# Kernel tuning notes

Hardware: AMD Instinct MI355X
Metric: run time of the kernel (lower is better)

Reference implementation:

```python
import jax, jax.numpy as jnp
import numpy as np

B, S, D, H, V, C = 4, 2048, 1024, 16, 32000, 10
FFN_DIM = 2 * D
HD = D // H
SCALE = float(np.sqrt(HD))


def _posenc(seq, d):
    pos = jnp.arange(seq, dtype=jnp.float32)[:, None]
    div = jnp.exp(jnp.arange(0, d, 2, dtype=jnp.float32) * (-np.log(10000.0) / d))
    pe = jnp.zeros((seq, d), dtype=jnp.float32)
    pe = pe.at[:, 0::2].set(jnp.sin(pos * div))
    pe = pe.at[:, 1::2].set(jnp.cos(pos * div))
    return pe


def _layernorm(x, g, b, eps=1e-5):
    mu = jnp.mean(x, axis=-1, keepdims=True)
    var = jnp.mean(jnp.square(x - mu), axis=-1, keepdims=True)
    return (x - mu) * jax.lax.rsqrt(var + eps) * g + b


def setup_inputs() -> dict:
    key = jax.random.key(0)
    ks = jax.random.split(key, 10)
    x_ids = jax.random.randint(ks[0], (B, S), 0, V, dtype=jnp.int64 if jax.config.jax_enable_x64 else jnp.int32)
    mask = jnp.ones((B, S), dtype=jnp.int32)
    emb = (jax.random.normal(ks[1], (V, D), jnp.float32) * 0.02).at[0].set(0.0)  # padding_idx=0
    qkv_w = jax.random.normal(ks[2], (3 * D, D), jnp.float32) * 0.02
    fc_w = jax.random.normal(ks[3], (D, D), jnp.float32) * 0.02
    fc_b = jnp.zeros((D,), jnp.float32)
    ln1_g = jnp.ones((D,), jnp.float32); ln1_b = jnp.zeros((D,), jnp.float32)
    ffn_w1 = jax.random.normal(ks[4], (FFN_DIM, D), jnp.float32) * 0.02
    ffn_b1 = jnp.zeros((FFN_DIM,), jnp.float32)
    ffn_w2 = jax.random.normal(ks[5], (D, FFN_DIM), jnp.float32) * 0.02
    ffn_b2 = jnp.zeros((D,), jnp.float32)
    ln2_g = jnp.ones((D,), jnp.float32); ln2_b = jnp.zeros((D,), jnp.float32)
    pr_w1 = jax.random.normal(ks[6], (D, D), jnp.float32) * 0.02
    pr_b1 = jnp.zeros((D,), jnp.float32)
    pr_w2 = jax.random.normal(ks[7], (C, D), jnp.float32) * 0.02
    pr_b2 = jnp.zeros((C,), jnp.float32)
    return dict(x_ids=x_ids, mask=mask, emb=emb, qkv_w=qkv_w, fc_w=fc_w, fc_b=fc_b,
                ln1_g=ln1_g, ln1_b=ln1_b, ffn_w1=ffn_w1, ffn_b1=ffn_b1,
                ffn_w2=ffn_w2, ffn_b2=ffn_b2, ln2_g=ln2_g, ln2_b=ln2_b,
                pr_w1=pr_w1, pr_b1=pr_b1, pr_w2=pr_w2, pr_b2=pr_b2)


def reference(x_ids, mask, emb, qkv_w, fc_w, fc_b, ln1_g, ln1_b,
              ffn_w1, ffn_b1, ffn_w2, ffn_b2, ln2_g, ln2_b,
              pr_w1, pr_b1, pr_w2, pr_b2):
    # embedding + absolute positional encoding
    x = emb[x_ids] + _posenc(S, D)  # [B,S,D]
    residual = x
    # multi-head attention (dropout is identity at eval)
    qkv = jnp.einsum('bsd,ed->bse', x, qkv_w)  # [B,S,3D]
    q, k, v = jnp.split(qkv, 3, axis=-1)
    q = q.reshape(B, S, H, HD)
    k = k.reshape(B, S, H, HD)
    v = v.reshape(B, S, H, HD)
    attn = jnp.einsum('bqhd,bkhd->bhqk', q, k) / SCALE  # [B,H,S,S]
    attn = jnp.where(mask[:, None, None, :] == 0, -jnp.inf, attn)
    attn = jax.nn.softmax(attn, axis=-1)
    o = jnp.einsum('bhqk,bkhd->bqhd', attn, v).reshape(B, S, D)
    o = jnp.einsum('bsd,ed->bse', o, fc_w) + fc_b
    x = _layernorm(o + residual, ln1_g, ln1_b)
    # FFN block (residual + LayerNorm inside)
    h = jax.nn.gelu(jnp.einsum('bsd,fd->bsf', x, ffn_w1) + ffn_b1, approximate=False)
    h = jnp.einsum('bsf,df->bsd', h, ffn_w2) + ffn_b2
    x = _layernorm(h + x, ln2_g, ln2_b)
    # masked max-pool over sequence
    x = jnp.where(mask[:, :, None] == 0, -jnp.inf, x).max(axis=1)  # [B,D]
    # prediction head
    h = jax.nn.gelu(x @ pr_w1.T + pr_b1, approximate=False)
    logits = h @ pr_w2.T + pr_b2  # [B,C]
    return logits
```

## Files before the change

### kernel.cpp

```cpp
#include <hip/hip_runtime.h>
#include <math.h>

#define B_   4
#define S_   2048
#define D_   1024
#define H_   16
#define HD_  64
#define C_   10
#define FFN_ 2048
#define M_   (B_ * S_)
#define D3_  (3 * D_)

typedef unsigned short u16;
typedef __bf16 bf16x8 __attribute__((ext_vector_type(8)));
typedef float  f32x4  __attribute__((ext_vector_type(4)));

__device__ __forceinline__ u16 f2bf(float f) {
  union { float f; unsigned u; } x; x.f = f;
  unsigned r = x.u + 0x7fffu + ((x.u >> 16) & 1u);
  return (u16)(r >> 16);
}
__device__ __forceinline__ unsigned pkbf(float a, float b) {
  union { float f; unsigned u; } x, y; x.f = a; y.f = b;
  return __builtin_amdgcn_perm(y.u + 0x8000u, x.u + 0x8000u, 0x07060302u);
}
__device__ __forceinline__ float gelu_f(float x) {
  return 0.5f * x * (1.f + erff(x * 0.70710678118654752440f));
}
__device__ __forceinline__ void gload_lds16(const void* g, void* l) {
  __builtin_amdgcn_global_load_lds(
      (const __attribute__((address_space(1))) unsigned int*)g,
      (__attribute__((address_space(3))) unsigned int*)l, 16, 0, 0);
}
__device__ __forceinline__ bf16x8 ldsfrag(const u16* buf, int rowbase, int fr, int kb) {
  return *(const bf16x8*)&buf[(rowbase + fr) * 64 + ((kb ^ (fr & 7)) << 3)];
}

__global__ __launch_bounds__(256) void cvt_kernel(const float* __restrict__ src,
                                                  u16* __restrict__ dst, int n) {
  const int i = (blockIdx.x * 256 + threadIdx.x) * 4;
  if (i >= n) return;
  f32x4 v = *(const f32x4*)&src[i];
  ushort4 o;
  o.x = f2bf(v[0]); o.y = f2bf(v[1]); o.z = f2bf(v[2]); o.w = f2bf(v[3]);
  *(ushort4*)&dst[i] = o;
}

__global__ __launch_bounds__(256) void embed_kernel(const int* __restrict__ ids,
                                                    const float* __restrict__ emb,
                                                    float* __restrict__ resid,
                                                    u16* __restrict__ xb) {
  const int m  = blockIdx.x;
  const int s  = m & (S_ - 1);
  const int id = ids[m];
  const int d0 = threadIdx.x * 4;
#pragma unroll
  for (int k = 0; k < 4; ++k) {
    const int d   = d0 + k;
    const float e = emb[(size_t)id * D_ + d];
    const float fr  = expf((float)(d & ~1) * (-9.210340371976184f / 1024.0f));
    const float ang = (float)s * fr;
    const float pe  = (d & 1) ? cosf(ang) : sinf(ang);
    const float v   = e + pe;
    resid[(size_t)m * D_ + d] = v;
    xb[(size_t)m * D_ + d]    = f2bf(v);
  }
}

template <int BIAS, int GELU, int OUTBF, int VSPLIT>
__global__ __launch_bounds__(256) void gemm_bt(const u16* __restrict__ A,
                                               const u16* __restrict__ W,
                                               const float* __restrict__ bias,
                                               float* __restrict__ outf,
                                               u16* __restrict__ outb,
                                               u16* __restrict__ vt,
                                               int M, int N, int K) {
  __shared__ u16 As[128 * 64];
  __shared__ u16 Bs[128 * 64];
  const int tid  = threadIdx.x;
  const int lane = tid & 63;
  const int w    = tid >> 6;
  const int bx   = blockIdx.x, by = blockIdx.y;
  const int l3   = lane >> 3;
  const int sb   = (lane & 7) ^ l3;
  const u16* Ag0 = A + (size_t)(by * 128 + w * 32 + l3) * K + sb * 8;
  const u16* Wg0 = W + (size_t)(bx * 128 + w * 32 + l3) * K + sb * 8;

  f32x4 acc[4][4] = {};
  const int wr  = (w & 1) * 64;
  const int wc  = (w >> 1) * 64;
  const int fr  = lane & 15;
  const int fq  = lane >> 4;

  for (int kt = 0; kt < K; kt += 64) {
#pragma unroll
    for (int c = 0; c < 4; ++c) {
      gload_lds16(Ag0 + (size_t)(c * 8) * K + kt, &As[(w * 32 + c * 8) * 64]);
      gload_lds16(Wg0 + (size_t)(c * 8) * K + kt, &Bs[(w * 32 + c * 8) * 64]);
    }
    __syncthreads();
#pragma unroll
    for (int ks = 0; ks < 2; ++ks) {
      const int kb = ks * 4 + fq;
      bf16x8 af[4], bfr[4];
#pragma unroll
      for (int i = 0; i < 4; ++i) af[i] = ldsfrag(As, wr + i * 16, fr, kb);
#pragma unroll
      for (int j = 0; j < 4; ++j) bfr[j] = ldsfrag(Bs, wc + j * 16, fr, kb);
#pragma unroll
      for (int i = 0; i < 4; ++i)
#pragma unroll
        for (int j = 0; j < 4; ++j)
          acc[i][j] = __builtin_amdgcn_mfma_f32_16x16x32_bf16(af[i], bfr[j], acc[i][j], 0, 0, 0);
    }
    __syncthreads();
  }

  const int er = fq * 4;
  const int ec = fr;
  if (VSPLIT && bx >= 16) {
#pragma unroll
    for (int i = 0; i < 4; ++i) {
      const int gm0 = by * 128 + wr + i * 16 + er;
      const int bb  = gm0 >> 11;
      const int s0  = gm0 & (S_ - 1);
#pragma unroll
      for (int j = 0; j < 4; ++j) {
        const int dcol = bx * 128 + wc + j * 16 + ec - 2 * D_;
        const int hh = dcol >> 6, dd = dcol & 63;
        ushort4 pk;
        pk.x = f2bf(acc[i][j][0]); pk.y = f2bf(acc[i][j][1]);
        pk.z = f2bf(acc[i][j][2]); pk.w = f2bf(acc[i][j][3]);
        *(ushort4*)&vt[((size_t)((bb * H_ + hh) * 64 + dd)) * S_ + s0] = pk;
      }
    }
    return;
  }
#pragma unroll
  for (int i = 0; i < 4; ++i) {
#pragma unroll
    for (int j = 0; j < 4; ++j) {
      const int gn = bx * 128 + wc + j * 16 + ec;
      const float bv = BIAS ? bias[gn] : 0.f;
#pragma unroll
      for (int r = 0; r < 4; ++r) {
        const int gm = by * 128 + wr + i * 16 + er + r;
        float v = acc[i][j][r] + bv;
        if (GELU) v = gelu_f(v);
        if (OUTBF) outb[(size_t)gm * N + gn] = f2bf(v);
        else       outf[(size_t)gm * N + gn] = v;
      }
    }
  }
}

#define EXPSCL 0.18033688011112042f

__global__ __launch_bounds__(256) void attn_mfma_kernel(const u16* __restrict__ qkv,
                                                        const u16* __restrict__ vt,
                                                        const int* __restrict__ mask,
                                                        u16* __restrict__ attno) {
  __shared__ u16 Qs[128 * 64];
  __shared__ u16 Ks[64 * 64];
  __shared__ u16 Vts[64 * 64];
  __shared__ u16 Ps[4][32 * 64];
  __shared__ float mb[64];
  const int tid = threadIdx.x, lane = tid & 63, w = tid >> 6;
  const int id = blockIdx.x;
  const int qt = (id >> 3) & 15;
  const int bh = (id & 7) * 8 + (id >> 7);
  const int b = bh >> 4, h = bh & 15;
  const int l3 = lane >> 3;
  const int sb = (lane & 7) ^ l3;
  const int fr = lane & 15, fq = lane >> 4;

  {
    const u16* qbase = qkv + (size_t)(b * S_ + qt * 128 + w * 32) * D3_ + h * 64 + sb * 8;
#pragma unroll
    for (int c = 0; c < 4; ++c)
      gload_lds16(qbase + (size_t)(c * 8 + l3) * D3_, &Qs[(w * 32 + c * 8) * 64]);
  }

  float m_st[2] = {-3e38f, -3e38f};
  float l_st[2] = {0.f, 0.f};
  f32x4 ot[4][2] = {};
  u16* PsW = Ps[w];

  for (int kt = 0; kt < S_ / 64; ++kt) {
    __syncthreads();
    {
      const u16* kbase = qkv + (size_t)(b * S_ + kt * 64 + w * 16) * D3_ + D_ + h * 64 + sb * 8;
      gload_lds16(kbase + (size_t)l3 * D3_, &Ks[(w * 16) * 64]);
      gload_lds16(kbase + (size_t)(8 + l3) * D3_, &Ks[(w * 16 + 8) * 64]);
      const u16* vbase = vt + ((size_t)((b * H_ + h) * 64 + w * 16)) * S_ + kt * 64 + sb * 8;
      gload_lds16(vbase + (size_t)l3 * S_, &Vts[(w * 16) * 64]);
      gload_lds16(vbase + (size_t)(8 + l3) * S_, &Vts[(w * 16 + 8) * 64]);
    }
    if (tid < 64) mb[tid] = (mask[b * S_ + kt * 64 + tid] != 0) ? 0.f : -1e30f;
    __syncthreads();

    f32x4 sf[4][2] = {};
#pragma unroll
    for (int ks = 0; ks < 2; ++ks) {
      const int kb = ks * 4 + fq;
      bf16x8 qf0 = ldsfrag(Qs, w * 32, fr, kb);
      bf16x8 qf1 = ldsfrag(Qs, w * 32 + 16, fr, kb);
#pragma unroll
      for (int r4 = 0; r4 < 4; ++r4) {
        bf16x8 kf = ldsfrag(Ks, r4 * 16, fr, kb);
        sf[r4][0] = __builtin_amdgcn_mfma_f32_16x16x32_bf16(kf, qf0, sf[r4][0], 0, 0, 0);
        sf[r4][1] = __builtin_amdgcn_mfma_f32_16x16x32_bf16(kf, qf1, sf[r4][1], 0, 0, 0);
      }
    }
#pragma unroll
    for (int r4 = 0; r4 < 4; ++r4) {
      const f32x4 vb = *(const f32x4*)&mb[r4 * 16 + fq * 4];
      sf[r4][0] += vb;
      sf[r4][1] += vb;
    }

#pragma unroll
    for (int i = 0; i < 2; ++i) {
      float mt = fmaxf(fmaxf(fmaxf(sf[0][i][0], sf[0][i][1]), fmaxf(sf[0][i][2], sf[0][i][3])),
                 fmaxf(fmaxf(fmaxf(sf[1][i][0], sf[1][i][1]), fmaxf(sf[1][i][2], sf[1][i][3])),
                 fmaxf(fmaxf(fmaxf(sf[2][i][0], sf[2][i][1]), fmaxf(sf[2][i][2], sf[2][i][3])),
                       fmaxf(fmaxf(sf[3][i][0], sf[3][i][1]), fmaxf(sf[3][i][2], sf[3][i][3])))));
      mt = fmaxf(mt, __shfl_xor(mt, 16));
      mt = fmaxf(mt, __shfl_xor(mt, 32));
      const float mo = m_st[i];
      const float mn = fmaxf(mo, mt);
      const float alpha = __builtin_exp2f((mo - mn) * EXPSCL);
      const int prow = i * 16 + fr;
      u16* pw = PsW + prow * 64;
      float sum = 0.f;
#pragma unroll
      for (int r4 = 0; r4 < 4; ++r4) {
        const float p0 = __builtin_exp2f((sf[r4][i][0] - mn) * EXPSCL);
        const float p1 = __builtin_exp2f((sf[r4][i][1] - mn) * EXPSCL);
        const float p2 = __builtin_exp2f((sf[r4][i][2] - mn) * EXPSCL);
        const float p3 = __builtin_exp2f((sf[r4][i][3] - mn) * EXPSCL);
        sum += (p0 + p1) + (p2 + p3);
        const int bk0 = 2 * r4 + (fq >> 1);
        const int off = ((bk0 ^ (prow & 7)) << 3) + ((fq & 1) << 2);
        uint2 pk; pk.x = pkbf(p0, p1); pk.y = pkbf(p2, p3);
        *(uint2*)&pw[off] = pk;
      }
      sum += __shfl_xor(sum, 16);
      sum += __shfl_xor(sum, 32);
      l_st[i] = l_st[i] * alpha + sum;
      m_st[i] = mn;
#pragma unroll
      for (int db = 0; db < 4; ++db) ot[db][i] *= alpha;
    }
    asm volatile("s_waitcnt lgkmcnt(0)" ::: "memory");

#pragma unroll
    for (int ks = 0; ks < 2; ++ks) {
      const int kb = ks * 4 + fq;
      bf16x8 pf0 = ldsfrag(PsW, 0, fr, kb);
      bf16x8 pf1 = ldsfrag(PsW, 16, fr, kb);
#pragma unroll
      for (int db = 0; db < 4; ++db) {
        bf16x8 vf = ldsfrag(Vts, db * 16, fr, kb);
        ot[db][0] = __builtin_amdgcn_mfma_f32_16x16x32_bf16(vf, pf0, ot[db][0], 0, 0, 0);
        ot[db][1] = __builtin_amdgcn_mfma_f32_16x16x32_bf16(vf, pf1, ot[db][1], 0, 0, 0);
      }
    }
  }

#pragma unroll
  for (int i = 0; i < 2; ++i) {
    const float l = l_st[i];
    const float inv = (l > 0.f) ? 1.f / l : 0.f;
    const int qrow = qt * 128 + w * 32 + i * 16 + fr;
    u16* dst = attno + (size_t)(b * S_ + qrow) * D_ + h * 64 + fq * 4;
#pragma unroll
    for (int db = 0; db < 4; ++db) {
      ushort4 pk;
      pk.x = f2bf(ot[db][i][0] * inv);
      pk.y = f2bf(ot[db][i][1] * inv);
      pk.z = f2bf(ot[db][i][2] * inv);
      pk.w = f2bf(ot[db][i][3] * inv);
      *(ushort4*)&dst[db * 16] = pk;
    }
  }
}

__global__ __launch_bounds__(256) void ln_kernel(const float* __restrict__ a,
                                                 const float* __restrict__ res,
                                                 const float* __restrict__ g,
                                                 const float* __restrict__ be,
                                                 float* __restrict__ outf,
                                                 u16* __restrict__ outb) {
  const int row = blockIdx.x, tid = threadIdx.x;
  const int lane = tid & 63, w = tid >> 6;
  const size_t base = (size_t)row * D_ + tid * 4;
  const f32x4 va = *(const f32x4*)(a + base);
  const f32x4 vr = *(const f32x4*)(res + base);
  const f32x4 v  = va + vr;
  float s = v[0] + v[1] + v[2] + v[3];
#pragma unroll
  for (int o = 32; o > 0; o >>= 1) s += __shfl_xor(s, o);
  __shared__ float red[8];
  if (lane == 0) red[w] = s;
  __syncthreads();
  const float mu = (red[0] + red[1] + red[2] + red[3]) * (1.f / D_);
  const f32x4 d = v - mu;
  float s2 = d[0] * d[0] + d[1] * d[1] + d[2] * d[2] + d[3] * d[3];
#pragma unroll
  for (int o = 32; o > 0; o >>= 1) s2 += __shfl_xor(s2, o);
  if (lane == 0) red[4 + w] = s2;
  __syncthreads();
  const float var = (red[4] + red[5] + red[6] + red[7]) * (1.f / D_);
  const float rs = rsqrtf(var + 1e-5f);
#pragma unroll
  for (int k = 0; k < 4; ++k) {
    const int ch = tid * 4 + k;
    const float y = d[k] * rs * g[ch] + be[ch];
    outf[base + k] = y;
    outb[base + k] = f2bf(y);
  }
}

__global__ __launch_bounds__(256) void pool_part_kernel(const float* __restrict__ x,
                                                        const int* __restrict__ mask,
                                                        float* __restrict__ part) {
  const int b = blockIdx.y, ch = blockIdx.x;
  const int d0 = threadIdx.x * 4;
  f32x4 acc = {-INFINITY, -INFINITY, -INFINITY, -INFINITY};
  for (int ss = 0; ss < 64; ++ss) {
    const int s = ch * 64 + ss;
    if (mask[b * S_ + s] != 0) {
      const f32x4 v = *(const f32x4*)&x[(size_t)(b * S_ + s) * D_ + d0];
      acc[0] = fmaxf(acc[0], v[0]);
      acc[1] = fmaxf(acc[1], v[1]);
      acc[2] = fmaxf(acc[2], v[2]);
      acc[3] = fmaxf(acc[3], v[3]);
    }
  }
  *(f32x4*)&part[(size_t)(b * 32 + ch) * D_ + d0] = acc;
}
__global__ __launch_bounds__(256) void pool_final_kernel(const float* __restrict__ part,
                                                         float* __restrict__ pooled) {
  const int b = blockIdx.x;
  const int d0 = threadIdx.x * 4;
  f32x4 acc = {-INFINITY, -INFINITY, -INFINITY, -INFINITY};
  for (int ch = 0; ch < 32; ++ch) {
    const f32x4 v = *(const f32x4*)&part[(size_t)(b * 32 + ch) * D_ + d0];
    acc[0] = fmaxf(acc[0], v[0]);
    acc[1] = fmaxf(acc[1], v[1]);
    acc[2] = fmaxf(acc[2], v[2]);
    acc[3] = fmaxf(acc[3], v[3]);
  }
  *(f32x4*)&pooled[(size_t)b * D_ + d0] = acc;
}

__global__ __launch_bounds__(256) void head1_kernel(const float* __restrict__ pooled,
                                                    const float* __restrict__ w,
                                                    const float* __restrict__ bias,
                                                    float* __restrict__ hh) {
  const int lane = threadIdx.x & 63;
  const int gw = blockIdx.x * 4 + (threadIdx.x >> 6);
  const int b = gw >> 10, n = gw & 1023;
  const float* p  = pooled + b * 1024;
  const float* wr = w + (size_t)n * 1024;
  float s = 0.f;
  for (int d = lane; d < 1024; d += 64) s += p[d] * wr[d];
#pragma unroll
  for (int off = 32; off > 0; off >>= 1) s += __shfl_xor(s, off);
  if (lane == 0) hh[b * 1024 + n] = gelu_f(s + bias[n]);
}
__global__ __launch_bounds__(256) void head2_kernel(const float* __restrict__ hh,
                                                    const float* __restrict__ w,
                                                    const float* __restrict__ bias,
                                                    float* __restrict__ out) {
  const int lane = threadIdx.x & 63;
  const int gw = blockIdx.x * 4 + (threadIdx.x >> 6);
  const int b = gw / 10, c = gw % 10;
  const float* p  = hh + b * 1024;
  const float* wr = w + (size_t)c * 1024;
  float s = 0.f;
  for (int d = lane; d < 1024; d += 64) s += p[d] * wr[d];
#pragma unroll
  for (int off = 32; off > 0; off >>= 1) s += __shfl_xor(s, off);
  if (lane == 0) out[b * 10 + c] = s + bias[c];
}

#define OFF_RESID  0UL
#define OFF_F1     33554432UL
#define OFF_XB     67108864UL
#define OFF_QKVB   83886080UL
#define OFF_ATTNO  134217728UL
#define OFF_WQKV   150994944UL
#define OFF_WFC    157286400UL
#define OFF_WF1    159383552UL
#define OFF_WF2    163577856UL
#define OFF_PART   167772160UL
#define OFF_POOLED 168296448UL
#define OFF_HH     168312832UL

extern "C" void kernel_launch(void* const* d_in, const int* in_sizes, int n_in,
                              void* d_out, int out_size, void* d_ws, size_t ws_size,
                              hipStream_t stream) {
  const int*   x_ids  = (const int*)d_in[0];
  const int*   mask   = (const int*)d_in[1];
  const float* emb    = (const float*)d_in[2];
  const float* qkv_w  = (const float*)d_in[3];
  const float* fc_w   = (const float*)d_in[4];
  const float* fc_b   = (const float*)d_in[5];
  const float* ln1_g  = (const float*)d_in[6];
  const float* ln1_b  = (const float*)d_in[7];
  const float* ffn_w1 = (const float*)d_in[8];
  const float* ffn_b1 = (const float*)d_in[9];
  const float* ffn_w2 = (const float*)d_in[10];
  const float* ffn_b2 = (const float*)d_in[11];
  const float* ln2_g  = (const float*)d_in[12];
  const float* ln2_b  = (const float*)d_in[13];
  const float* pr_w1  = (const float*)d_in[14];
  const float* pr_b1  = (const float*)d_in[15];
  const float* pr_w2  = (const float*)d_in[16];
  const float* pr_b2  = (const float*)d_in[17];
  float* out = (float*)d_out;
  char* ws = (char*)d_ws;

  float* resid  = (float*)(ws + OFF_RESID);
  float* f1     = (float*)(ws + OFF_F1);
  u16*   vtb    = (u16*)(ws + OFF_F1);
  u16*   xb     = (u16*)(ws + OFF_XB);
  u16*   qkvb   = (u16*)(ws + OFF_QKVB);
  u16*   hb     = (u16*)(ws + OFF_QKVB);
  u16*   attnob = (u16*)(ws + OFF_ATTNO);
  u16*   wqkvb  = (u16*)(ws + OFF_WQKV);
  u16*   wfcb   = (u16*)(ws + OFF_WFC);
  u16*   wf1b   = (u16*)(ws + OFF_WF1);
  u16*   wf2b   = (u16*)(ws + OFF_WF2);
  float* part   = (float*)(ws + OFF_PART);
  float* pooled = (float*)(ws + OFF_POOLED);
  float* hh     = (float*)(ws + OFF_HH);

  cvt_kernel<<<3072, 256, 0, stream>>>(qkv_w,  wqkvb, 3 * D_ * D_);
  cvt_kernel<<<1024, 256, 0, stream>>>(fc_w,   wfcb,  D_ * D_);
  cvt_kernel<<<2048, 256, 0, stream>>>(ffn_w1, wf1b,  FFN_ * D_);
  cvt_kernel<<<2048, 256, 0, stream>>>(ffn_w2, wf2b,  D_ * FFN_);

  embed_kernel<<<M_, 256, 0, stream>>>(x_ids, emb, resid, xb);

  gemm_bt<0, 0, 1, 1><<<dim3(D3_ / 128, M_ / 128), 256, 0, stream>>>(
      xb, wqkvb, nullptr, nullptr, qkvb, vtb, M_, D3_, D_);

  attn_mfma_kernel<<<1024, 256, 0, stream>>>(qkvb, vtb, mask, attnob);

  gemm_bt<1, 0, 0, 0><<<dim3(D_ / 128, M_ / 128), 256, 0, stream>>>(
      attnob, wfcb, fc_b, f1, nullptr, nullptr, M_, D_, D_);

  ln_kernel<<<M_, 256, 0, stream>>>(f1, resid, ln1_g, ln1_b, resid, xb);

  gemm_bt<1, 1, 1, 0><<<dim3(FFN_ / 128, M_ / 128), 256, 0, stream>>>(
      xb, wf1b, ffn_b1, nullptr, hb, nullptr, M_, FFN_, D_);

  gemm_bt<1, 0, 0, 0><<<dim3(D_ / 128, M_ / 128), 256, 0, stream>>>(
      hb, wf2b, ffn_b2, f1, nullptr, nullptr, M_, D_, FFN_);

  ln_kernel<<<M_, 256, 0, stream>>>(f1, resid, ln2_g, ln2_b, f1, xb);

  pool_part_kernel<<<dim3(32, B_), 256, 0, stream>>>(f1, mask, part);
  pool_final_kernel<<<B_, 256, 0, stream>>>(part, pooled);

  head1_kernel<<<1024, 256, 0, stream>>>(pooled, pr_w1, pr_b1, hh);
  head2_kernel<<<10, 256, 0, stream>>>(hh, pr_w2, pr_b2, out);
}
```

Baseline: 669.1 us.

## Fuse weight casts, vectorize GEMM epilogue, skip full-mask bias, trim LN writes

Merges the four weight-conversion launches into one kernel. Swaps the MFMA operand order so each lane holds four consecutive output columns, which allows vectorized bias loads and 16-byte or 8-byte epilogue stores; the transposed V write becomes strided scalar stores as a result. The attention kernel now uses a 3D grid instead of the swizzled block index and checks once whether the whole mask row is valid, skipping the per-tile mask bias when it is. The final LayerNorm no longer writes an unused bf16 copy, and its fp32 output is stored as vectors.

```diff
diff --git a/kernel.cpp b/kernel.cpp
--- a/kernel.cpp
+++ b/kernel.cpp
@@ -36,14 +36,29 @@
   return *(const bf16x8*)&buf[(rowbase + fr) * 64 + ((kb ^ (fr & 7)) << 3)];
 }
 
-__global__ __launch_bounds__(256) void cvt_kernel(const float* __restrict__ src,
-                                                  u16* __restrict__ dst, int n) {
-  const int i = (blockIdx.x * 256 + threadIdx.x) * 4;
-  if (i >= n) return;
-  f32x4 v = *(const f32x4*)&src[i];
+#define CV0 786432
+#define CV1 262144
+#define CV2 524288
+#define CV3 524288
+__global__ __launch_bounds__(256) void cvt4_kernel(const float* __restrict__ s0,
+                                                   const float* __restrict__ s1,
+                                                   const float* __restrict__ s2,
+                                                   const float* __restrict__ s3,
+                                                   u16* __restrict__ d0,
+                                                   u16* __restrict__ d1,
+                                                   u16* __restrict__ d2,
+                                                   u16* __restrict__ d3) {
+  int v = blockIdx.x * 256 + threadIdx.x;
+  const float* s; u16* d;
+  if (v < CV0) { s = s0; d = d0; }
+  else if (v < CV0 + CV1) { s = s1; d = d1; v -= CV0; }
+  else if (v < CV0 + CV1 + CV2) { s = s2; d = d2; v -= CV0 + CV1; }
+  else { s = s3; d = d3; v -= CV0 + CV1 + CV2; }
+  const int i = v * 4;
+  f32x4 x = *(const f32x4*)&s[i];
   ushort4 o;
-  o.x = f2bf(v[0]); o.y = f2bf(v[1]); o.z = f2bf(v[2]); o.w = f2bf(v[3]);
-  *(ushort4*)&dst[i] = o;
+  o.x = f2bf(x[0]); o.y = f2bf(x[1]); o.z = f2bf(x[2]); o.w = f2bf(x[3]);
+  *(ushort4*)&d[i] = o;
 }
 
 __global__ __launch_bounds__(256) void embed_kernel(const int* __restrict__ ids,
@@ -111,44 +126,45 @@
       for (int i = 0; i < 4; ++i)
 #pragma unroll
         for (int j = 0; j < 4; ++j)
-          acc[i][j] = __builtin_amdgcn_mfma_f32_16x16x32_bf16(af[i], bfr[j], acc[i][j], 0, 0, 0);
+          acc[i][j] = __builtin_amdgcn_mfma_f32_16x16x32_bf16(bfr[j], af[i], acc[i][j], 0, 0, 0);
     }
     __syncthreads();
   }
 
-  const int er = fq * 4;
-  const int ec = fr;
   if (VSPLIT && bx >= 16) {
 #pragma unroll
     for (int i = 0; i < 4; ++i) {
-      const int gm0 = by * 128 + wr + i * 16 + er;
-      const int bb  = gm0 >> 11;
-      const int s0  = gm0 & (S_ - 1);
+      const int m = by * 128 + wr + i * 16 + fr;
+      const int bb = m >> 11, s0 = m & (S_ - 1);
 #pragma unroll
       for (int j = 0; j < 4; ++j) {
-        const int dcol = bx * 128 + wc + j * 16 + ec - 2 * D_;
-        const int hh = dcol >> 6, dd = dcol & 63;
+        const int d0c = bx * 128 + wc + j * 16 + fq * 4 - 2 * D_;
+        const int hh = d0c >> 6, dd = d0c & 63;
+        u16* vdst = &vt[((size_t)((bb * H_ + hh) * 64 + dd)) * S_ + s0];
+#pragma unroll
+        for (int r = 0; r < 4; ++r) vdst[(size_t)r * S_] = f2bf(acc[i][j][r]);
+      }
+    }
+    return;
+  }
+#pragma unroll
+  for (int i = 0; i < 4; ++i) {
+    const int m = by * 128 + wr + i * 16 + fr;
+#pragma unroll
+    for (int j = 0; j < 4; ++j) {
+      const int nb = bx * 128 + wc + j * 16 + fq * 4;
+      f32x4 v = acc[i][j];
+      if (BIAS) v += *(const f32x4*)&bias[nb];
+      if (GELU) {
+        v[0] = gelu_f(v[0]); v[1] = gelu_f(v[1]);
+        v[2] = gelu_f(v[2]); v[3] = gelu_f(v[3]);
+      }
+      if (OUTBF) {
         ushort4 pk;
-        pk.x = f2bf(acc[i][j][0]); pk.y = f2bf(acc[i][j][1]);
-        pk.z = f2bf(acc[i][j][2]); pk.w = f2bf(acc[i][j][3]);
-        *(ushort4*)&vt[((size_t)((bb * H_ + hh) * 64 + dd)) * S_ + s0] = pk;
-      }
-    }
-    return;
-  }
-#pragma unroll
-  for (int i = 0; i < 4; ++i) {
-#pragma unroll
-    for (int j = 0; j < 4; ++j) {
-      const int gn = bx * 128 + wc + j * 16 + ec;
-      const float bv = BIAS ? bias[gn] : 0.f;
-#pragma unroll
-      for (int r = 0; r < 4; ++r) {
-        const int gm = by * 128 + wr + i * 16 + er + r;
-        float v = acc[i][j][r] + bv;
-        if (GELU) v = gelu_f(v);
-        if (OUTBF) outb[(size_t)gm * N + gn] = f2bf(v);
-        else       outf[(size_t)gm * N + gn] = v;
+        pk.x = f2bf(v[0]); pk.y = f2bf(v[1]); pk.z = f2bf(v[2]); pk.w = f2bf(v[3]);
+        *(ushort4*)&outb[(size_t)m * N + nb] = pk;
+      } else {
+        *(f32x4*)&outf[(size_t)m * N + nb] = v;
       }
     }
   }
@@ -165,11 +181,9 @@
   __shared__ u16 Vts[64 * 64];
   __shared__ u16 Ps[4][32 * 64];
   __shared__ float mb[64];
+  __shared__ int allv_s;
   const int tid = threadIdx.x, lane = tid & 63, w = tid >> 6;
-  const int id = blockIdx.x;
-  const int qt = (id >> 3) & 15;
-  const int bh = (id & 7) * 8 + (id >> 7);
-  const int b = bh >> 4, h = bh & 15;
+  const int qt = blockIdx.x, h = blockIdx.y, b = blockIdx.z;
   const int l3 = lane >> 3;
   const int sb = (lane & 7) ^ l3;
   const int fr = lane & 15, fq = lane >> 4;
@@ -180,6 +194,18 @@
     for (int c = 0; c < 4; ++c)
       gload_lds16(qbase + (size_t)(c * 8 + l3) * D3_, &Qs[(w * 32 + c * 8) * 64]);
   }
+  if (tid == 0) allv_s = 1;
+  __syncthreads();
+  {
+    int mv = 1;
+#pragma unroll
+    for (int s0 = 0; s0 < 8; ++s0) mv &= (mask[b * S_ + s0 * 256 + tid] != 0);
+    if (__ballot(mv != 0) != ~0ull) {
+      if (lane == 0) atomicAnd(&allv_s, 0);
+    }
+  }
+  __syncthreads();
+  const bool ALLV = (allv_s != 0);
 
   float m_st[2] = {-3e38f, -3e38f};
   float l_st[2] = {0.f, 0.f};
@@ -196,7 +222,7 @@
       gload_lds16(vbase + (size_t)l3 * S_, &Vts[(w * 16) * 64]);
       gload_lds16(vbase + (size_t)(8 + l3) * S_, &Vts[(w * 16 + 8) * 64]);
     }
-    if (tid < 64) mb[tid] = (mask[b * S_ + kt * 64 + tid] != 0) ? 0.f : -1e30f;
+    if (!ALLV && tid < 64) mb[tid] = (mask[b * S_ + kt * 64 + tid] != 0) ? 0.f : -1e30f;
     __syncthreads();
 
     f32x4 sf[4][2] = {};
@@ -212,11 +238,13 @@
         sf[r4][1] = __builtin_amdgcn_mfma_f32_16x16x32_bf16(kf, qf1, sf[r4][1], 0, 0, 0);
       }
     }
-#pragma unroll
-    for (int r4 = 0; r4 < 4; ++r4) {
-      const f32x4 vb = *(const f32x4*)&mb[r4 * 16 + fq * 4];
-      sf[r4][0] += vb;
-      sf[r4][1] += vb;
+    if (!ALLV) {
+#pragma unroll
+      for (int r4 = 0; r4 < 4; ++r4) {
+        const f32x4 vb = *(const f32x4*)&mb[r4 * 16 + fq * 4];
+        sf[r4][0] += vb;
+        sf[r4][1] += vb;
+      }
     }
 
 #pragma unroll
@@ -286,6 +314,7 @@
   }
 }
 
+template <int WRITEB>
 __global__ __launch_bounds__(256) void ln_kernel(const float* __restrict__ a,
                                                  const float* __restrict__ res,
                                                  const float* __restrict__ g,
@@ -313,12 +342,17 @@
   __syncthreads();
   const float var = (red[4] + red[5] + red[6] + red[7]) * (1.f / D_);
   const float rs = rsqrtf(var + 1e-5f);
+  f32x4 y;
+  ushort4 pk;
 #pragma unroll
   for (int k = 0; k < 4; ++k) {
     const int ch = tid * 4 + k;
-    const float y = d[k] * rs * g[ch] + be[ch];
-    outf[base + k] = y;
-    outb[base + k] = f2bf(y);
+    y[k] = d[k] * rs * g[ch] + be[ch];
+  }
+  *(f32x4*)&outf[base] = y;
+  if (WRITEB) {
+    pk.x = f2bf(y[0]); pk.y = f2bf(y[1]); pk.z = f2bf(y[2]); pk.w = f2bf(y[3]);
+    *(ushort4*)&outb[base] = pk;
   }
 }
 
@@ -438,22 +472,20 @@
   float* pooled = (float*)(ws + OFF_POOLED);
   float* hh     = (float*)(ws + OFF_HH);
 
-  cvt_kernel<<<3072, 256, 0, stream>>>(qkv_w,  wqkvb, 3 * D_ * D_);
-  cvt_kernel<<<1024, 256, 0, stream>>>(fc_w,   wfcb,  D_ * D_);
-  cvt_kernel<<<2048, 256, 0, stream>>>(ffn_w1, wf1b,  FFN_ * D_);
-  cvt_kernel<<<2048, 256, 0, stream>>>(ffn_w2, wf2b,  D_ * FFN_);
+  cvt4_kernel<<<8192, 256, 0, stream>>>(qkv_w, fc_w, ffn_w1, ffn_w2,
+                                        wqkvb, wfcb, wf1b, wf2b);
 
   embed_kernel<<<M_, 256, 0, stream>>>(x_ids, emb, resid, xb);
 
   gemm_bt<0, 0, 1, 1><<<dim3(D3_ / 128, M_ / 128), 256, 0, stream>>>(
       xb, wqkvb, nullptr, nullptr, qkvb, vtb, M_, D3_, D_);
 
-  attn_mfma_kernel<<<1024, 256, 0, stream>>>(qkvb, vtb, mask, attnob);
+  attn_mfma_kernel<<<dim3(S_ / 128, H_, B_), 256, 0, stream>>>(qkvb, vtb, mask, attnob);
 
   gemm_bt<1, 0, 0, 0><<<dim3(D_ / 128, M_ / 128), 256, 0, stream>>>(
       attnob, wfcb, fc_b, f1, nullptr, nullptr, M_, D_, D_);
 
-  ln_kernel<<<M_, 256, 0, stream>>>(f1, resid, ln1_g, ln1_b, resid, xb);
+  ln_kernel<1><<<M_, 256, 0, stream>>>(f1, resid, ln1_g, ln1_b, resid, xb);
 
   gemm_bt<1, 1, 1, 0><<<dim3(FFN_ / 128, M_ / 128), 256, 0, stream>>>(
       xb, wf1b, ffn_b1, nullptr, hb, nullptr, M_, FFN_, D_);
@@ -461,7 +493,7 @@
   gemm_bt<1, 0, 0, 0><<<dim3(D_ / 128, M_ / 128), 256, 0, stream>>>(
       hb, wf2b, ffn_b2, f1, nullptr, nullptr, M_, D_, FFN_);
 
-  ln_kernel<<<M_, 256, 0, stream>>>(f1, resid, ln2_g, ln2_b, f1, xb);
+  ln_kernel<0><<<M_, 256, 0, stream>>>(f1, resid, ln2_g, ln2_b, f1, nullptr);
 
   pool_part_kernel<<<dim3(32, B_), 256, 0, stream>>>(f1, mask, part);
   pool_final_kernel<<<B_, 256, 0, stream>>>(part, pooled);
```

Result: no change. 667.4 us (-0.3%).
